# Performance work log

Hardware: AMD Instinct MI355X
Metric: run time of the kernel (lower is better)

The kernel has to match this reference:

```python
import jax, jax.numpy as jnp
import numpy as np

N = 100000; E = 1600000; G = 256
DIMS = [16, 64, 128, 128, 64]
HEADS = 4


def _self_loops(edge_index, n):
    loop = jnp.arange(n, dtype=edge_index.dtype)
    row = jnp.concatenate([edge_index[0], loop])  # source nodes j
    col = jnp.concatenate([edge_index[1], loop])  # target nodes i (aggregation index)
    return row, col


def _gcn(x, row, col, W, b, n):
    deg = jax.ops.segment_sum(jnp.ones_like(col, jnp.float32), col, num_segments=n)
    dis = jax.lax.rsqrt(deg)  # self-loops guarantee deg >= 1
    norm = dis[row] * dis[col]  # [E+N]
    h = x @ W  # [N, dout]
    return jax.ops.segment_sum(h[row] * norm[:, None], col, num_segments=n) + b


def _gat(x, row, col, W, a_src, a_dst, b, n):
    # PyG GATConv with self-loops; per-edge softmax over incoming neighborhoods.
    H, C = a_src.shape
    h = (x @ W).reshape(n, H, C)
    asrc = jnp.einsum('nhc,hc->nh', h, a_src)
    adst = jnp.einsum('nhc,hc->nh', h, a_dst)
    e = jax.nn.leaky_relu(asrc[row] + adst[col], 0.2)  # [E+N, H]
    m = jax.ops.segment_max(e, col, num_segments=n)
    ex = jnp.exp(e - m[col])
    s = jax.ops.segment_sum(ex, col, num_segments=n)
    alpha = ex / s[col]  # segment softmax over edges sharing a target
    out = jax.ops.segment_sum(h[row] * alpha[..., None], col, num_segments=n)
    return out.reshape(n, H * C) + b  # heads concatenated so residual add is valid


def _bn(x, g, b):
    # BatchNorm1d training-mode normalization (biased variance), eps=1e-5
    mu = jnp.mean(x, 0)
    var = jnp.var(x, 0)
    return (x - mu) * jax.lax.rsqrt(var + 1e-5) * g + b


def _forward(x, edge_index, batch, p):
    row, col = _self_loops(edge_index, N)
    gat_at = {0: 0, 2: 1}  # layers 0 and 2 have attention (i % 2 == 0 and i < n-1)
    n_layers = len(DIMS) - 1
    for i in range(n_layers):
        x = _gcn(x, row, col, p['gcn_w'][i], p['gcn_b'][i], N)
        x = _bn(x, p['bn_g'][i], p['bn_b'][i])
        if i in gat_at:
            j = gat_at[i]
            x = _gat(x, row, col, p['gat_w'][j], p['gat_asrc'][j], p['gat_adst'][j], p['gat_b'][j], N) + x
        if i < n_layers - 1:
            x = jax.nn.leaky_relu(x, 0.2)
            # dropout: identity in eval mode
    sums = jax.ops.segment_sum(x, batch, num_segments=G)
    cnt = jax.ops.segment_sum(jnp.ones((N,), jnp.float32), batch, num_segments=G)
    return sums / jnp.maximum(cnt, 1.0)[:, None]  # global_mean_pool -> [G, latent]


def setup_inputs() -> dict:
    key = jax.random.key(0)
    ks = jax.random.split(key, 16)
    inp = {}
    inp['x'] = jax.random.normal(ks[0], (N, DIMS[0]), jnp.float32)
    inp['edge_index'] = jax.random.randint(ks[1], (2, E), 0, N, dtype=jnp.int32)
    inp['batch'] = jnp.sort(jax.random.randint(ks[2], (N,), 0, G, dtype=jnp.int32))
    k = 3
    for i in range(4):
        din, dout = DIMS[i], DIMS[i + 1]
        inp[f'gcn_w{i}'] = jax.random.normal(ks[k], (din, dout), jnp.float32) / np.sqrt(din).astype(np.float32); k += 1
        inp[f'gcn_b{i}'] = jnp.zeros((dout,), jnp.float32)
        inp[f'bn_g{i}'] = jnp.ones((dout,), jnp.float32)
        inp[f'bn_b{i}'] = jnp.zeros((dout,), jnp.float32)
    for i in (0, 2):
        d = DIMS[i + 1]; C = d // HEADS
        inp[f'gat_w{i}'] = jax.random.normal(ks[k], (d, d), jnp.float32) / np.sqrt(d).astype(np.float32); k += 1
        inp[f'gat_asrc{i}'] = jax.random.normal(ks[k], (HEADS, C), jnp.float32) * 0.1; k += 1
        inp[f'gat_adst{i}'] = jax.random.normal(ks[k], (HEADS, C), jnp.float32) * 0.1; k += 1
        inp[f'gat_b{i}'] = jnp.zeros((d,), jnp.float32)
    return inp


def reference(x, edge_index, batch,
              gcn_w0, gcn_b0, bn_g0, bn_b0,
              gcn_w1, gcn_b1, bn_g1, bn_b1,
              gcn_w2, gcn_b2, bn_g2, bn_b2,
              gcn_w3, gcn_b3, bn_g3, bn_b3,
              gat_w0, gat_asrc0, gat_adst0, gat_b0,
              gat_w2, gat_asrc2, gat_adst2, gat_b2):
    p = {
        'gcn_w': [gcn_w0, gcn_w1, gcn_w2, gcn_w3],
        'gcn_b': [gcn_b0, gcn_b1, gcn_b2, gcn_b3],
        'bn_g': [bn_g0, bn_g1, bn_g2, bn_g3],
        'bn_b': [bn_b0, bn_b1, bn_b2, bn_b3],
        'gat_w': [gat_w0, gat_w2],
        'gat_asrc': [gat_asrc0, gat_asrc2],
        'gat_adst': [gat_adst0, gat_adst2],
        'gat_b': [gat_b0, gat_b2],
    }
    return _forward(x, edge_index, batch, p)
```

## Files before the change

kernel.cpp:

```cpp
#include <hip/hip_runtime.h>

static constexpr int GRAPHS = 256;
static constexpr int SCAN_CHUNK = 1024;
static constexpr int XCDS = 8;
static constexpr int SREP = 8;

typedef _Float16 h16;
typedef _Float16 h16x2 __attribute__((ext_vector_type(2)));
typedef _Float16 h16x4 __attribute__((ext_vector_type(4)));
typedef _Float16 v8h __attribute__((ext_vector_type(8)));
typedef float v4f __attribute__((ext_vector_type(4)));

__device__ __forceinline__ float lrelu(float v) { return fmaxf(v, 0.2f * v); }
__device__ __forceinline__ int rfl(int v) { return __builtin_amdgcn_readfirstlane(v); }

__global__ void zero_f32_kernel(float* __restrict__ p, int n) {
  int i = blockIdx.x * blockDim.x + threadIdx.x;
  if (i < n) p[i] = 0.0f;
}

__global__ void init_counts_kernel(int* __restrict__ cnt, int n) {
  int i = blockIdx.x * blockDim.x + threadIdx.x;
  if (i < n) cnt[i] = 1;
}

__global__ void count_edges_kernel(const int* __restrict__ ei, int* __restrict__ cnt, int E) {
  int e = blockIdx.x * blockDim.x + threadIdx.x;
  if (e < E) atomicAdd(&cnt[ei[E + e]], 1);
}

__global__ void block_sum_kernel(const int* __restrict__ counts, int* __restrict__ partial,
                                 int n) {
  __shared__ int sh[256];
  int base = blockIdx.x * SCAN_CHUNK;
  int t = threadIdx.x;
  int lim = min(base + SCAN_CHUNK, n);
  int s = 0;
  for (int i = base + t; i < lim; i += 256) s += counts[i];
  sh[t] = s;
  __syncthreads();
  for (int off = 128; off > 0; off >>= 1) {
    if (t < off) sh[t] += sh[t + off];
    __syncthreads();
  }
  if (t == 0) partial[blockIdx.x] = sh[0];
}

__global__ void partial_scan_kernel(int* __restrict__ partial, int* __restrict__ rowptr,
                                    int nblocks, int n) {
  __shared__ int sh[256];
  int t = threadIdx.x;
  int v = (t < nblocks) ? partial[t] : 0;
  sh[t] = v;
  __syncthreads();
  for (int off = 1; off < 256; off <<= 1) {
    int u = (t >= off) ? sh[t - off] : 0;
    __syncthreads();
    sh[t] += u;
    __syncthreads();
  }
  if (t < nblocks) partial[t] = sh[t] - v;
  if (t == 255) rowptr[n] = sh[255];
}

__global__ void chunk_scan_kernel(const int* __restrict__ counts, const int* __restrict__ partial,
                                  int* __restrict__ rowptr, int n) {
  __shared__ int sh[256];
  int base = blockIdx.x * SCAN_CHUNK;
  int t = threadIdx.x;
  int i0 = base + t * 4;
  int c0 = 0, c1 = 0, c2 = 0, c3 = 0;
  if (i0 + 3 < n) {
    int4 c = *(const int4*)(counts + i0);
    c0 = c.x;
    c1 = c.y;
    c2 = c.z;
    c3 = c.w;
  } else {
    if (i0 < n) c0 = counts[i0];
    if (i0 + 1 < n) c1 = counts[i0 + 1];
    if (i0 + 2 < n) c2 = counts[i0 + 2];
  }
  int tot = c0 + c1 + c2 + c3;
  sh[t] = tot;
  __syncthreads();
  for (int off = 1; off < 256; off <<= 1) {
    int u = (t >= off) ? sh[t - off] : 0;
    __syncthreads();
    sh[t] += u;
    __syncthreads();
  }
  int run = partial[blockIdx.x] + sh[t] - tot;
  if (i0 < n) { rowptr[i0] = run; run += c0; }
  if (i0 + 1 < n) { rowptr[i0 + 1] = run; run += c1; }
  if (i0 + 2 < n) { rowptr[i0 + 2] = run; run += c2; }
  if (i0 + 3 < n) { rowptr[i0 + 3] = run; }
}

__global__ void finalize_csr_kernel(const int* __restrict__ rowptr, float* __restrict__ dis,
                                    int* __restrict__ cursor, int* __restrict__ csr, int n) {
  int i = blockIdx.x * blockDim.x + threadIdx.x;
  if (i >= n) return;
  int s = rowptr[i], e = rowptr[i + 1];
  dis[i] = rsqrtf((float)(e - s));
  csr[s] = i;
  cursor[i] = s + 1;
}

__global__ void fill_edges_kernel(const int* __restrict__ ei, int* __restrict__ cursor,
                                  int* __restrict__ csr, int E, int nb) {
  int p = blockIdx.x & (XCDS - 1);
  int lo = p * nb, hi = lo + nb;
  int nchunks = gridDim.x >> 3;
  int chunk = blockIdx.x >> 3;
  int stride = nchunks * blockDim.x;
  for (int e = chunk * blockDim.x + threadIdx.x; e < E; e += stride) {
    int c = ei[E + e];
    if (c >= lo && c < hi) {
      int pos = atomicAdd(&cursor[c], 1);
      csr[pos] = ei[e];
    }
  }
}

template <int K, int N>
__global__ void wt_kernel(const float* __restrict__ W, h16* __restrict__ WT) {
  int gid = blockIdx.x * blockDim.x + threadIdx.x;
  if (gid >= K * N) return;
  int k = gid / N, n = gid % N;
  WT[n * K + k] = (h16)W[gid];
}

template <int K, int N, bool STATS>
__global__ void gemm_mfma_kernel(const h16* __restrict__ x, const h16* __restrict__ WT,
                                 const float* __restrict__ bias, const float* __restrict__ coefIn,
                                 h16* __restrict__ out, double* __restrict__ stats, int n_nodes) {
  constexpr int KP = K + 8;
  constexpr int NT = N / 16;
  __shared__ h16 Ah[128 * KP];
  __shared__ h16 Bs[N * KP];
  __shared__ float sh1[N], sh2[N];
  int tid = threadIdx.x;
  int node0 = blockIdx.x * 128;
  int limit = min(128, n_nodes - node0);
  if (STATS && tid < N) {
    sh1[tid] = 0.f;
    sh2[tid] = 0.f;
  }
  for (int i = tid; i < 128 * (K / 8); i += 256) {
    int row = i / (K / 8), kb = i % (K / 8);
    v8h v = {};
    if (row < limit) {
      v = *(const v8h*)(x + (size_t)(node0 + row) * K + kb * 8);
      if (coefIn) {
#pragma unroll
        for (int j = 0; j < 8; ++j)
          v[j] = (h16)fmaf((float)v[j], coefIn[kb * 8 + j], coefIn[K + kb * 8 + j]);
      }
    }
    *(v8h*)(Ah + row * KP + kb * 8) = v;
  }
  for (int i = tid; i < N * (K / 8); i += 256) {
    int nrow = i / (K / 8), kb = i % (K / 8);
    *(v8h*)(Bs + nrow * KP + kb * 8) = *(const v8h*)(WT + (size_t)nrow * K + kb * 8);
  }
  __syncthreads();

  int w = tid >> 6, lane = tid & 63, quad = lane >> 4, l16 = lane & 15;
  v4f acc[2][NT];
#pragma unroll
  for (int rt = 0; rt < 2; ++rt)
#pragma unroll
    for (int nt = 0; nt < NT; ++nt) acc[rt][nt] = (v4f){0.f, 0.f, 0.f, 0.f};

  int rowb = w * 32;
#pragma unroll
  for (int ks = 0; ks < K / 32; ++ks) {
    v8h a0 = *(const v8h*)(Ah + (rowb + l16) * KP + ks * 32 + quad * 8);
    v8h a1 = *(const v8h*)(Ah + (rowb + 16 + l16) * KP + ks * 32 + quad * 8);
#pragma unroll
    for (int nt = 0; nt < NT; ++nt) {
      v8h b = *(const v8h*)(Bs + (nt * 16 + l16) * KP + ks * 32 + quad * 8);
      acc[0][nt] = __builtin_amdgcn_mfma_f32_16x16x32_f16(a0, b, acc[0][nt], 0, 0, 0);
      acc[1][nt] = __builtin_amdgcn_mfma_f32_16x16x32_f16(a1, b, acc[1][nt], 0, 0, 0);
    }
  }

#pragma unroll
  for (int nt = 0; nt < NT; ++nt) {
    int col = nt * 16 + l16;
    float bv = bias ? bias[col] : 0.f;
    float p1 = 0.f, p2 = 0.f;
#pragma unroll
    for (int rt = 0; rt < 2; ++rt) {
#pragma unroll
      for (int reg = 0; reg < 4; ++reg) {
        int row = rowb + rt * 16 + quad * 4 + reg;
        if (row < limit) {
          float v = acc[rt][nt][reg] + bv;
          out[(size_t)(node0 + row) * N + col] = (h16)v;
          if (STATS) {
            p1 += v;
            p2 = fmaf(v, v, p2);
          }
        }
      }
    }
    if (STATS) {
      atomicAdd(&sh1[col], p1);
      atomicAdd(&sh2[col], p2);
    }
  }
  if (STATS) {
    __syncthreads();
    double* st = stats + (blockIdx.x & (SREP - 1)) * 256;
    if (tid < N) {
      atomicAdd(&st[tid], (double)sh1[tid]);
      atomicAdd(&st[N + tid], (double)sh2[tid]);
    }
  }
}

template <int K, int DOUT, int MT, bool STATS>
__global__ void gemm_tile_kernel(const h16* __restrict__ x, const float* __restrict__ W,
                                 const float* __restrict__ bias, h16* __restrict__ out,
                                 double* __restrict__ stats, int n_nodes) {
  constexpr int COLG = DOUT / 4;
  constexpr int ROWG = 256 / COLG;
  constexpr int NODES = ROWG * MT;
  constexpr int KP = K + 4;
  __shared__ float xs[NODES * KP];
  __shared__ float sh1[DOUT], sh2[DOUT];
  int tid = threadIdx.x;
  if (STATS && tid < DOUT) {
    sh1[tid] = 0.f;
    sh2[tid] = 0.f;
  }
  int node0 = blockIdx.x * NODES;
  int limit = min(NODES, n_nodes - node0);
  const h16x4* src = (const h16x4*)(x + (size_t)node0 * K);
  int tile_q = (limit * K) >> 2;
  for (int i = tid; i < tile_q; i += 256) {
    h16x4 v = src[i];
    int row = i / (K / 4), cq = i % (K / 4);
    float4 f;
    f.x = (float)v[0];
    f.y = (float)v[1];
    f.z = (float)v[2];
    f.w = (float)v[3];
    *(float4*)(xs + row * KP + cq * 4) = f;
  }
  __syncthreads();
  int cg = tid % COLG, rg = tid / COLG;
  int c0 = cg * 4;
  float acc[MT][4];
#pragma unroll
  for (int m = 0; m < MT; ++m)
#pragma unroll
    for (int i = 0; i < 4; ++i) acc[m][i] = 0.f;

  for (int k4 = 0; k4 < K / 4; ++k4) {
    int k = k4 * 4;
    float4 w0 = *(const float4*)(W + (size_t)(k + 0) * DOUT + c0);
    float4 w1 = *(const float4*)(W + (size_t)(k + 1) * DOUT + c0);
    float4 w2 = *(const float4*)(W + (size_t)(k + 2) * DOUT + c0);
    float4 w3 = *(const float4*)(W + (size_t)(k + 3) * DOUT + c0);
#pragma unroll
    for (int m = 0; m < MT; ++m) {
      float4 xv = *(const float4*)(xs + (rg * MT + m) * KP + k);
      acc[m][0] = fmaf(xv.x, w0.x, acc[m][0]);
      acc[m][1] = fmaf(xv.x, w0.y, acc[m][1]);
      acc[m][2] = fmaf(xv.x, w0.z, acc[m][2]);
      acc[m][3] = fmaf(xv.x, w0.w, acc[m][3]);
      acc[m][0] = fmaf(xv.y, w1.x, acc[m][0]);
      acc[m][1] = fmaf(xv.y, w1.y, acc[m][1]);
      acc[m][2] = fmaf(xv.y, w1.z, acc[m][2]);
      acc[m][3] = fmaf(xv.y, w1.w, acc[m][3]);
      acc[m][0] = fmaf(xv.z, w2.x, acc[m][0]);
      acc[m][1] = fmaf(xv.z, w2.y, acc[m][1]);
      acc[m][2] = fmaf(xv.z, w2.z, acc[m][2]);
      acc[m][3] = fmaf(xv.z, w2.w, acc[m][3]);
      acc[m][0] = fmaf(xv.w, w3.x, acc[m][0]);
      acc[m][1] = fmaf(xv.w, w3.y, acc[m][1]);
      acc[m][2] = fmaf(xv.w, w3.z, acc[m][2]);
      acc[m][3] = fmaf(xv.w, w3.w, acc[m][3]);
    }
  }
  float4 bv = make_float4(0.f, 0.f, 0.f, 0.f);
  if (bias) bv = *(const float4*)(bias + c0);
  float p1[4] = {0.f, 0.f, 0.f, 0.f}, p2[4] = {0.f, 0.f, 0.f, 0.f};
#pragma unroll
  for (int m = 0; m < MT; ++m) {
    int node = node0 + rg * MT + m;
    if (node < n_nodes) {
      float v0 = acc[m][0] + bv.x, v1 = acc[m][1] + bv.y;
      float v2 = acc[m][2] + bv.z, v3 = acc[m][3] + bv.w;
      h16x4 r;
      r[0] = (h16)v0;
      r[1] = (h16)v1;
      r[2] = (h16)v2;
      r[3] = (h16)v3;
      *(h16x4*)(out + (size_t)node * DOUT + c0) = r;
      if (STATS) {
        p1[0] += v0;
        p1[1] += v1;
        p1[2] += v2;
        p1[3] += v3;
        p2[0] = fmaf(v0, v0, p2[0]);
        p2[1] = fmaf(v1, v1, p2[1]);
        p2[2] = fmaf(v2, v2, p2[2]);
        p2[3] = fmaf(v3, v3, p2[3]);
      }
    }
  }
  if (STATS) {
#pragma unroll
    for (int i = 0; i < 4; ++i) {
      atomicAdd(&sh1[c0 + i], p1[i]);
      atomicAdd(&sh2[c0 + i], p2[i]);
    }
    __syncthreads();
    double* st = stats + (blockIdx.x & (SREP - 1)) * 256;
    if (tid < DOUT) {
      atomicAdd(&st[tid], (double)sh1[tid]);
      atomicAdd(&st[DOUT + tid], (double)sh2[tid]);
    }
  }
}

template <int D>
__global__ void bn_stats_kernel(const h16* __restrict__ x, double* __restrict__ stats, int n) {
  int tid = threadIdx.x;
  int c = tid & (D - 1);
  const int rpb = 256 / D;
  float s1 = 0.f, s2 = 0.f;
  for (int r = blockIdx.x * rpb + tid / D; r < n; r += gridDim.x * rpb) {
    float v = (float)x[(size_t)r * D + c];
    s1 += v;
    s2 = fmaf(v, v, s2);
  }
  double* st = stats + (blockIdx.x & (SREP - 1)) * 256;
  atomicAdd(&st[c], (double)s1);
  atomicAdd(&st[D + c], (double)s2);
}

template <int D>
__global__ void bn_coef_kernel(const double* __restrict__ stats, const float* __restrict__ g,
                               const float* __restrict__ b, float* __restrict__ coef, int n) {
  int c = threadIdx.x;
  if (c >= D) return;
  double s1 = 0.0, s2 = 0.0;
#pragma unroll
  for (int r = 0; r < SREP; ++r) {
    s1 += stats[r * 256 + c];
    s2 += stats[r * 256 + D + c];
  }
  double inv_n = 1.0 / (double)n;
  double mu = s1 * inv_n;
  double var = s2 * inv_n - mu * mu;
  float A = (float)(1.0 / sqrt(var + 1e-5)) * g[c];
  coef[c] = A;
  coef[D + c] = b[c] - (float)mu * A;
}

__global__ void gcn_agg16_kernel(const float* __restrict__ h, const int* __restrict__ rowptr,
                                 const int* __restrict__ csr, const float* __restrict__ dis,
                                 h16* __restrict__ out, int n) {
  int wave = (blockIdx.x * blockDim.x + threadIdx.x) >> 6;
  int lane = threadIdx.x & 63;
  if (wave >= n) return;
  int s = rowptr[wave], e = rowptr[wave + 1];
  int q = lane >> 4, c = lane & 15;
  float acc = 0.f;
  for (int k = s + q; k < e; k += 4) {
    int j = csr[k];
    acc = fmaf(dis[j], h[(size_t)j * 16 + c], acc);
  }
  acc += __shfl_xor(acc, 16, 64);
  acc += __shfl_xor(acc, 32, 64);
  if (lane < 16) out[(size_t)wave * 16 + lane] = (h16)(dis[wave] * acc);
}

__global__ void gcn_agg64_kernel(const h16* __restrict__ h, const int* __restrict__ rowptr,
                                 const int* __restrict__ csr, const float* __restrict__ dis,
                                 const float* __restrict__ bias, h16* __restrict__ out, int n) {
  int wave = (blockIdx.x * blockDim.x + threadIdx.x) >> 6;
  int lane = threadIdx.x & 63;
  if (wave >= n) return;
  int s = rfl(rowptr[wave]);
  int e = rfl(rowptr[wave + 1]);
  float a[4] = {0.f, 0.f, 0.f, 0.f};
  int k = s;
  for (; k + 8 <= e; k += 8) {
    int j[8];
    float d[8];
#pragma unroll
    for (int u = 0; u < 8; ++u) j[u] = rfl(csr[k + u]);
#pragma unroll
    for (int u = 0; u < 8; ++u) d[u] = dis[j[u]];
#pragma unroll
    for (int u = 0; u < 8; ++u) {
      const h16* rp = h + (size_t)j[u] * 64;
      a[u & 3] = fmaf(d[u], (float)rp[lane], a[u & 3]);
    }
  }
  for (; k + 4 <= e; k += 4) {
    int j[4];
#pragma unroll
    for (int u = 0; u < 4; ++u) j[u] = rfl(csr[k + u]);
#pragma unroll
    for (int u = 0; u < 4; ++u) {
      const h16* rp = h + (size_t)j[u] * 64;
      a[u] = fmaf(dis[j[u]], (float)rp[lane], a[u]);
    }
  }
  for (; k < e; ++k) {
    int j0 = rfl(csr[k]);
    const h16* rp = h + (size_t)j0 * 64;
    a[0] = fmaf(dis[j0], (float)rp[lane], a[0]);
  }
  float b0 = bias ? bias[lane] : 0.f;
  out[(size_t)wave * 64 + lane] = (h16)fmaf(dis[wave], (a[0] + a[1]) + (a[2] + a[3]), b0);
}

template <bool COEF>
__global__ void gcn_agg128_kernel(const h16* __restrict__ h, const int* __restrict__ rowptr,
                                  const int* __restrict__ csr, const float* __restrict__ dis,
                                  const float* __restrict__ coef, h16* __restrict__ out, int n) {
  int wave = (blockIdx.x * blockDim.x + threadIdx.x) >> 6;
  int lane = threadIdx.x & 63;
  if (wave >= n) return;
  int s = rfl(rowptr[wave]);
  int e = rfl(rowptr[wave + 1]);
  int c2 = lane * 2;
  float2 A2 = make_float2(0.f, 0.f), B2 = make_float2(0.f, 0.f);
  if (COEF) {
    A2 = *(const float2*)(coef + c2);
    B2 = *(const float2*)(coef + 128 + c2);
  }
  float a0[4] = {0.f, 0.f, 0.f, 0.f};
  float a1[4] = {0.f, 0.f, 0.f, 0.f};
  int k = s;
  for (; k + 8 <= e; k += 8) {
    int j[8];
    float d[8];
#pragma unroll
    for (int u = 0; u < 8; ++u) j[u] = rfl(csr[k + u]);
#pragma unroll
    for (int u = 0; u < 8; ++u) d[u] = dis[j[u]];
#pragma unroll
    for (int u = 0; u < 8; ++u) {
      const h16* rp = h + (size_t)j[u] * 128;
      h16x2 v = *(const h16x2*)(rp + c2);
      float f0 = (float)v[0], f1 = (float)v[1];
      if (COEF) {
        f0 = lrelu(fmaf(f0, A2.x, B2.x));
        f1 = lrelu(fmaf(f1, A2.y, B2.y));
      }
      a0[u & 3] = fmaf(d[u], f0, a0[u & 3]);
      a1[u & 3] = fmaf(d[u], f1, a1[u & 3]);
    }
  }
  for (; k < e; ++k) {
    int j0 = rfl(csr[k]);
    float d0 = dis[j0];
    const h16* rp = h + (size_t)j0 * 128;
    h16x2 v = *(const h16x2*)(rp + c2);
    float f0 = (float)v[0], f1 = (float)v[1];
    if (COEF) {
      f0 = lrelu(fmaf(f0, A2.x, B2.x));
      f1 = lrelu(fmaf(f1, A2.y, B2.y));
    }
    a0[0] = fmaf(d0, f0, a0[0]);
    a1[0] = fmaf(d0, f1, a1[0]);
  }
  float di = dis[wave];
  h16x2 r;
  r[0] = (h16)(di * ((a0[0] + a0[1]) + (a0[2] + a0[3])));
  r[1] = (h16)(di * ((a1[0] + a1[1]) + (a1[2] + a1[3])));
  *(h16x2*)(out + (size_t)wave * 128 + c2) = r;
}

template <int C>
__global__ void att_coef_kernel(const h16* __restrict__ h2, const float* __restrict__ a_src,
                                const float* __restrict__ a_dst, float* __restrict__ asrc,
                                float* __restrict__ adst, int n) {
  int gid = blockIdx.x * blockDim.x + threadIdx.x;
  if (gid >= n * 4) return;
  int nd = gid >> 2, h = gid & 3;
  const h16* hr = h2 + (size_t)nd * 4 * C + h * C;
  float s1 = 0.f, s2 = 0.f;
#pragma unroll
  for (int c = 0; c < C; ++c) {
    float v = (float)hr[c];
    s1 = fmaf(v, a_src[h * C + c], s1);
    s2 = fmaf(v, a_dst[h * C + c], s2);
  }
  asrc[gid] = s1;
  adst[gid] = s2;
}

__global__ void edge_coef_kernel(const int* __restrict__ rowptr, const int* __restrict__ csr,
                                 const float* __restrict__ asrc, const float* __restrict__ adst,
                                 float* __restrict__ exbuf, float* __restrict__ dinv, int n) {
  int wave = (blockIdx.x * blockDim.x + threadIdx.x) >> 6;
  int lane = threadIdx.x & 63;
  if (wave >= n) return;
  int h = lane & 3, es = lane >> 2;
  float ad = adst[wave * 4 + h];
  int s = rowptr[wave], e = rowptr[wave + 1];
  float den = 0.f;
  for (int k = s + es; k < e; k += 16) {
    int j = csr[k];
    float v = __expf(lrelu(asrc[j * 4 + h] + ad));
    exbuf[(size_t)k * 4 + h] = v;
    den += v;
  }
  den += __shfl_xor(den, 4, 64);
  den += __shfl_xor(den, 8, 64);
  den += __shfl_xor(den, 16, 64);
  den += __shfl_xor(den, 32, 64);
  if (lane < 4) dinv[wave * 4 + h] = 1.0f / den;
}

__global__ void gat_agg64_kernel(const h16* __restrict__ h2, const int* __restrict__ rowptr,
                                 const int* __restrict__ csr, const float* __restrict__ exbuf,
                                 const float* __restrict__ dinv, const float* __restrict__ bias,
                                 const h16* __restrict__ xres, const float* __restrict__ rescoef,
                                 h16* __restrict__ out, int n) {
  int wave = (blockIdx.x * blockDim.x + threadIdx.x) >> 6;
  int lane = threadIdx.x & 63;
  if (wave >= n) return;
  int head = lane >> 4;
  int s = rfl(rowptr[wave]);
  int e = rfl(rowptr[wave + 1]);
  float a[4] = {0.f, 0.f, 0.f, 0.f};
  int k = s;
  for (; k + 8 <= e; k += 8) {
    int j[8];
    float ex[8];
#pragma unroll
    for (int u = 0; u < 8; ++u) {
      j[u] = rfl(csr[k + u]);
      ex[u] = exbuf[(size_t)(k + u) * 4 + head];
    }
#pragma unroll
    for (int u = 0; u < 8; ++u) {
      const h16* rp = h2 + (size_t)j[u] * 64;
      a[u & 3] = fmaf(ex[u], (float)rp[lane], a[u & 3]);
    }
  }
  for (; k + 4 <= e; k += 4) {
    int j[4];
    float ex[4];
#pragma unroll
    for (int u = 0; u < 4; ++u) {
      j[u] = rfl(csr[k + u]);
      ex[u] = exbuf[(size_t)(k + u) * 4 + head];
    }
#pragma unroll
    for (int u = 0; u < 4; ++u) {
      const h16* rp = h2 + (size_t)j[u] * 64;
      a[u] = fmaf(ex[u], (float)rp[lane], a[u]);
    }
  }
  for (; k < e; ++k) {
    int j0 = rfl(csr[k]);
    const h16* rp = h2 + (size_t)j0 * 64;
    a[0] = fmaf(exbuf[(size_t)k * 4 + head], (float)rp[lane], a[0]);
  }
  float dv = dinv[wave * 4 + head];
  size_t base = (size_t)wave * 64;
  float xv = fmaf((float)xres[base + lane], rescoef[lane], rescoef[64 + lane]);
  float v0 = ((a[0] + a[1]) + (a[2] + a[3])) * dv + bias[lane] + xv;
  out[base + lane] = (h16)lrelu(v0);
}

__global__ void gat_agg128_kernel(const h16* __restrict__ h2, const int* __restrict__ rowptr,
                                  const int* __restrict__ csr, const float* __restrict__ exbuf,
                                  const float* __restrict__ dinv, const float* __restrict__ bias,
                                  const h16* __restrict__ xres, const float* __restrict__ rescoef,
                                  h16* __restrict__ out, int n) {
  int wave = (blockIdx.x * blockDim.x + threadIdx.x) >> 6;
  int lane = threadIdx.x & 63;
  if (wave >= n) return;
  int head = lane >> 4;
  int c2 = lane * 2;
  int s = rfl(rowptr[wave]);
  int e = rfl(rowptr[wave + 1]);
  float a0[4] = {0.f, 0.f, 0.f, 0.f};
  float a1[4] = {0.f, 0.f, 0.f, 0.f};
  int k = s;
  for (; k + 8 <= e; k += 8) {
    int j[8];
    float ex[8];
#pragma unroll
    for (int u = 0; u < 8; ++u) {
      j[u] = rfl(csr[k + u]);
      ex[u] = exbuf[(size_t)(k + u) * 4 + head];
    }
#pragma unroll
    for (int u = 0; u < 8; ++u) {
      const h16* rp = h2 + (size_t)j[u] * 128;
      h16x2 v = *(const h16x2*)(rp + c2);
      a0[u & 3] = fmaf(ex[u], (float)v[0], a0[u & 3]);
      a1[u & 3] = fmaf(ex[u], (float)v[1], a1[u & 3]);
    }
  }
  for (; k + 4 <= e; k += 4) {
    int j[4];
    float ex[4];
#pragma unroll
    for (int u = 0; u < 4; ++u) {
      j[u] = rfl(csr[k + u]);
      ex[u] = exbuf[(size_t)(k + u) * 4 + head];
    }
#pragma unroll
    for (int u = 0; u < 4; ++u) {
      const h16* rp = h2 + (size_t)j[u] * 128;
      h16x2 v = *(const h16x2*)(rp + c2);
      a0[u] = fmaf(ex[u], (float)v[0], a0[u]);
      a1[u] = fmaf(ex[u], (float)v[1], a1[u]);
    }
  }
  for (; k < e; ++k) {
    int j0 = rfl(csr[k]);
    float e0 = exbuf[(size_t)k * 4 + head];
    const h16* rp = h2 + (size_t)j0 * 128;
    h16x2 v = *(const h16x2*)(rp + c2);
    a0[0] = fmaf(e0, (float)v[0], a0[0]);
    a1[0] = fmaf(e0, (float)v[1], a1[0]);
  }
  float dv = dinv[wave * 4 + head];
  float2 b2 = *(const float2*)(bias + c2);
  float2 A2 = *(const float2*)(rescoef + c2);
  float2 B2 = *(const float2*)(rescoef + 128 + c2);
  size_t base = (size_t)wave * 128;
  h16x2 xr = *(const h16x2*)(xres + base + c2);
  float xr0 = fmaf((float)xr[0], A2.x, B2.x);
  float xr1 = fmaf((float)xr[1], A2.y, B2.y);
  float v0 = ((a0[0] + a0[1]) + (a0[2] + a0[3])) * dv + b2.x + xr0;
  float v1 = ((a1[0] + a1[1]) + (a1[2] + a1[3])) * dv + b2.y + xr1;
  h16x2 r;
  r[0] = (h16)lrelu(v0);
  r[1] = (h16)lrelu(v1);
  *(h16x2*)(out + base + c2) = r;
}

__global__ void graph_bounds_kernel(const int* __restrict__ batch, int* __restrict__ bounds,
                                    int n) {
  int g = threadIdx.x;
  if (g >= GRAPHS) return;
  int lo = 0, hi = n;
  while (lo < hi) {
    int mid = (lo + hi) >> 1;
    if (batch[mid] < g)
      lo = mid + 1;
    else
      hi = mid;
  }
  bounds[g] = lo;
  if (g == 0) bounds[GRAPHS] = n;
}

__global__ void pool_kernel(const h16* __restrict__ x, const int* __restrict__ bounds,
                            const float* __restrict__ coef, float* __restrict__ out) {
  __shared__ float sh[4][64];
  int g = blockIdx.x;
  int lane = threadIdx.x & 63, w = threadIdx.x >> 6;
  int s = bounds[g], e = bounds[g + 1];
  float acc = 0.f;
  for (int r = s + w; r < e; r += 4) acc += (float)x[(size_t)r * 64 + lane];
  sh[w][lane] = acc;
  __syncthreads();
  if (w == 0) {
    float t = sh[0][lane] + sh[1][lane] + sh[2][lane] + sh[3][lane];
    float cntf = (float)(e - s);
    out[(g << 6) + lane] = fmaf(coef[lane], t, coef[64 + lane] * cntf) / fmaxf(cntf, 1.0f);
  }
}

extern "C" void kernel_launch(void* const* d_in, const int* in_sizes, int n_in, void* d_out,
                              int out_size, void* d_ws, size_t ws_size, hipStream_t stream) {
  const float* x_in = (const float*)d_in[0];
  const int* ei = (const int*)d_in[1];
  const int* batch = (const int*)d_in[2];
  const float* gcn_w[4] = {(const float*)d_in[3], (const float*)d_in[7], (const float*)d_in[11],
                           (const float*)d_in[15]};
  const float* gcn_b[4] = {(const float*)d_in[4], (const float*)d_in[8], (const float*)d_in[12],
                           (const float*)d_in[16]};
  const float* bn_g[4] = {(const float*)d_in[5], (const float*)d_in[9], (const float*)d_in[13],
                          (const float*)d_in[17]};
  const float* bn_b[4] = {(const float*)d_in[6], (const float*)d_in[10], (const float*)d_in[14],
                          (const float*)d_in[18]};
  const float* gat_w0 = (const float*)d_in[19];
  const float* gat_as0 = (const float*)d_in[20];
  const float* gat_ad0 = (const float*)d_in[21];
  const float* gat_b0 = (const float*)d_in[22];
  const float* gat_w2 = (const float*)d_in[23];
  const float* gat_as2 = (const float*)d_in[24];
  const float* gat_ad2 = (const float*)d_in[25];
  const float* gat_b2 = (const float*)d_in[26];

  const int N = in_sizes[2];
  const int E = in_sizes[1] / 2;

  char* wp = (char*)d_ws;
  auto alloc = [&](size_t bytes) -> void* {
    void* p = (void*)wp;
    wp += (bytes + 255) & ~(size_t)255;
    return p;
  };
  double* statsAll = (double*)alloc(4 * SREP * 256 * sizeof(double));
  float* coefAll = (float*)alloc(4 * 256 * sizeof(float));
  int* rowptr = (int*)alloc((size_t)(N + 1) * 4);
  int* cursor = (int*)alloc((size_t)N * 4);
  int* partial = (int*)alloc(256 * sizeof(int));
  int* csr = (int*)alloc((size_t)(N + E) * 4);
  float* dis = (float*)alloc((size_t)N * 4);
  h16* bufA = (h16*)alloc((size_t)N * 128 * 2);
  h16* bufB = (h16*)alloc((size_t)N * 128 * 2);
  h16* bufC = (h16*)alloc((size_t)N * 128 * 2);
  float* attS = (float*)alloc((size_t)N * 4 * 4);
  float* attD = (float*)alloc((size_t)N * 4 * 4);
  float* exbuf = (float*)alloc((size_t)(N + E) * 4 * 4);
  float* dinv = (float*)alloc((size_t)N * 4 * 4);
  int* bounds = (int*)alloc((size_t)(GRAPHS + 1) * 4);
  h16* wt0 = (h16*)alloc(64 * 64 * 2);
  h16* wt1 = (h16*)alloc(64 * 128 * 2);
  h16* wt2 = (h16*)alloc(128 * 128 * 2);
  h16* wt3 = (h16*)alloc(128 * 128 * 2);
  h16* wt4 = (h16*)alloc(128 * 64 * 2);
  if ((size_t)(wp - (char*)d_ws) > ws_size) return;

  double* stats0 = statsAll;
  double* stats1 = statsAll + SREP * 256;
  double* stats2 = statsAll + 2 * SREP * 256;
  double* stats3 = statsAll + 3 * SREP * 256;
  float* coef0 = coefAll;
  float* coef1 = coefAll + 256;
  float* coef2 = coefAll + 512;
  float* coef3 = coefAll + 768;

  const int B = 256;
  auto cd = [](int a, int b) { return (a + b - 1) / b; };
  const int scan_blocks = cd(N, SCAN_CHUNK);

  zero_f32_kernel<<<cd(4 * SREP * 512, B), B, 0, stream>>>((float*)statsAll, 4 * SREP * 512);
  wt_kernel<64, 64><<<cd(64 * 64, B), B, 0, stream>>>(gat_w0, wt0);
  wt_kernel<64, 128><<<cd(64 * 128, B), B, 0, stream>>>(gcn_w[1], wt1);
  wt_kernel<128, 128><<<cd(128 * 128, B), B, 0, stream>>>(gcn_w[2], wt2);
  wt_kernel<128, 128><<<cd(128 * 128, B), B, 0, stream>>>(gat_w2, wt3);
  wt_kernel<128, 64><<<cd(128 * 64, B), B, 0, stream>>>(gcn_w[3], wt4);
  init_counts_kernel<<<cd(N, B), B, 0, stream>>>(cursor, N);
  count_edges_kernel<<<cd(E, B), B, 0, stream>>>(ei, cursor, E);
  block_sum_kernel<<<scan_blocks, B, 0, stream>>>(cursor, partial, N);
  partial_scan_kernel<<<1, B, 0, stream>>>(partial, rowptr, scan_blocks, N);
  chunk_scan_kernel<<<scan_blocks, B, 0, stream>>>(cursor, partial, rowptr, N);
  finalize_csr_kernel<<<cd(N, B), B, 0, stream>>>(rowptr, dis, cursor, csr, N);
  {
    int nb = cd(N, XCDS);
    fill_edges_kernel<<<XCDS * 512, B, 0, stream>>>(ei, cursor, csr, E, nb);
  }
  graph_bounds_kernel<<<1, 256, 0, stream>>>(batch, bounds, N);

  gcn_agg16_kernel<<<cd(N * 64, B), B, 0, stream>>>(x_in, rowptr, csr, dis, bufB, N);
  gemm_tile_kernel<16, 64, 8, true>
      <<<cd(N, 128), B, 0, stream>>>(bufB, gcn_w[0], gcn_b[0], bufC, stats0, N);
  bn_coef_kernel<64><<<1, 64, 0, stream>>>(stats0, bn_g[0], bn_b[0], coef0, N);
  gemm_mfma_kernel<64, 64, false>
      <<<cd(N, 128), B, 0, stream>>>(bufC, wt0, nullptr, coef0, bufB, nullptr, N);
  att_coef_kernel<16><<<cd(N * 4, B), B, 0, stream>>>(bufB, gat_as0, gat_ad0, attS, attD, N);
  edge_coef_kernel<<<cd(N * 64, B), B, 0, stream>>>(rowptr, csr, attS, attD, exbuf, dinv, N);
  gat_agg64_kernel<<<cd(N * 64, B), B, 0, stream>>>(bufB, rowptr, csr, exbuf, dinv, gat_b0, bufC,
                                                    coef0, bufA, N);

  gcn_agg64_kernel<<<cd(N * 64, B), B, 0, stream>>>(bufA, rowptr, csr, dis, nullptr, bufB, N);
  gemm_mfma_kernel<64, 128, true>
      <<<cd(N, 128), B, 0, stream>>>(bufB, wt1, gcn_b[1], nullptr, bufC, stats1, N);
  bn_coef_kernel<128><<<1, 128, 0, stream>>>(stats1, bn_g[1], bn_b[1], coef1, N);

  gcn_agg128_kernel<true><<<cd(N * 64, B), B, 0, stream>>>(bufC, rowptr, csr, dis, coef1, bufB, N);
  gemm_mfma_kernel<128, 128, true>
      <<<cd(N, 128), B, 0, stream>>>(bufB, wt2, gcn_b[2], nullptr, bufA, stats2, N);
  bn_coef_kernel<128><<<1, 128, 0, stream>>>(stats2, bn_g[2], bn_b[2], coef2, N);
  gemm_mfma_kernel<128, 128, false>
      <<<cd(N, 128), B, 0, stream>>>(bufA, wt3, nullptr, coef2, bufB, nullptr, N);
  att_coef_kernel<32><<<cd(N * 4, B), B, 0, stream>>>(bufB, gat_as2, gat_ad2, attS, attD, N);
  edge_coef_kernel<<<cd(N * 64, B), B, 0, stream>>>(rowptr, csr, attS, attD, exbuf, dinv, N);
  gat_agg128_kernel<<<cd(N * 64, B), B, 0, stream>>>(bufB, rowptr, csr, exbuf, dinv, gat_b2, bufA,
                                                     coef2, bufC, N);

  gemm_mfma_kernel<128, 64, false>
      <<<cd(N, 128), B, 0, stream>>>(bufC, wt4, nullptr, nullptr, bufB, nullptr, N);
  gcn_agg64_kernel<<<cd(N * 64, B), B, 0, stream>>>(bufB, rowptr, csr, dis, gcn_b[3], bufA, N);
  bn_stats_kernel<64><<<256, 256, 0, stream>>>(bufA, stats3, N);
  bn_coef_kernel<64><<<1, 64, 0, stream>>>(stats3, bn_g[3], bn_b[3], coef3, N);

  pool_kernel<<<GRAPHS, 256, 0, stream>>>(bufA, bounds, coef3, (float*)d_out);
}
```

Measured before the change: 915.8 us.

## Fuse GAT edge softmax into aggregation and bucket edges by target partition

Removes the separate edge_coef kernel and its exbuf/dinv buffers. Each GAT aggregation wave now computes the exp-scores for 8 edges at once across 32 lanes, broadcasts them with shuffles, and accumulates the softmax denominator inline. CSR construction now first partitions edges into 8 target-range buckets through a histogram, prefix and scatter, so the count and fill atomics touch only a contiguous slice per XCD instead of each partition rescanning all edges. This avoids writing and rereading the per-edge coefficient buffer and the 8x redundant edge-list scans, at the cost of an extra scatter pass through an 8-byte-per-edge staging buffer.

```diff
diff --git a/kernel.cpp b/kernel.cpp
--- a/kernel.cpp
+++ b/kernel.cpp
@@ -24,9 +24,64 @@
   if (i < n) cnt[i] = 1;
 }
 
-__global__ void count_edges_kernel(const int* __restrict__ ei, int* __restrict__ cnt, int E) {
-  int e = blockIdx.x * blockDim.x + threadIdx.x;
-  if (e < E) atomicAdd(&cnt[ei[E + e]], 1);
+__global__ void bucket_hist_kernel(const int* __restrict__ ei, int* __restrict__ bcnt, int E,
+                                   int nbkt) {
+  __shared__ int h[8];
+  if (threadIdx.x < 8) h[threadIdx.x] = 0;
+  __syncthreads();
+  int stride = gridDim.x * blockDim.x;
+  for (int e = blockIdx.x * blockDim.x + threadIdx.x; e < E; e += stride)
+    atomicAdd(&h[ei[E + e] / nbkt], 1);
+  __syncthreads();
+  if (threadIdx.x < 8) atomicAdd(&bcnt[threadIdx.x], h[threadIdx.x]);
+}
+
+__global__ void bucket_prefix_kernel(const int* __restrict__ bcnt, int* __restrict__ bstart,
+                                     int* __restrict__ bcursor) {
+  int run = 0;
+  for (int i = 0; i < 8; ++i) {
+    bstart[i] = run;
+    bcursor[i] = run;
+    run += bcnt[i];
+  }
+  bstart[8] = run;
+}
+
+__global__ void bucket_scatter_kernel(const int* __restrict__ ei, int* __restrict__ bcursor,
+                                      int2* __restrict__ ebuf, int E, int nbkt) {
+  constexpr int EPT = 8;
+  __shared__ int h[8], base[8];
+  int tid = threadIdx.x;
+  if (tid < 8) h[tid] = 0;
+  __syncthreads();
+  int base_e = blockIdx.x * (256 * EPT);
+  int src[EPT], tgt[EPT], bk[EPT], rnk[EPT];
+#pragma unroll
+  for (int i = 0; i < EPT; ++i) {
+    int e = base_e + i * 256 + tid;
+    bk[i] = -1;
+    if (e < E) {
+      tgt[i] = ei[E + e];
+      src[i] = ei[e];
+      bk[i] = tgt[i] / nbkt;
+      rnk[i] = atomicAdd(&h[bk[i]], 1);
+    }
+  }
+  __syncthreads();
+  if (tid < 8) base[tid] = atomicAdd(&bcursor[tid], h[tid]);
+  __syncthreads();
+#pragma unroll
+  for (int i = 0; i < EPT; ++i)
+    if (bk[i] >= 0) ebuf[base[bk[i]] + rnk[i]] = make_int2(src[i], tgt[i]);
+}
+
+__global__ void count_bucket_kernel(const int2* __restrict__ ebuf, const int* __restrict__ bstart,
+                                    int* __restrict__ cnt) {
+  int p = blockIdx.x & (XCDS - 1);
+  int s = bstart[p], e = bstart[p + 1];
+  int ch = blockIdx.x >> 3, nch = gridDim.x >> 3;
+  int stride = nch * 256;
+  for (int i = s + ch * 256 + threadIdx.x; i < e; i += stride) atomicAdd(&cnt[ebuf[i].y], 1);
 }
 
 __global__ void block_sum_kernel(const int* __restrict__ counts, int* __restrict__ partial,
@@ -107,19 +162,16 @@
   cursor[i] = s + 1;
 }
 
-__global__ void fill_edges_kernel(const int* __restrict__ ei, int* __restrict__ cursor,
-                                  int* __restrict__ csr, int E, int nb) {
+__global__ void fill_bucket_kernel(const int2* __restrict__ ebuf, const int* __restrict__ bstart,
+                                   int* __restrict__ cursor, int* __restrict__ csr) {
   int p = blockIdx.x & (XCDS - 1);
-  int lo = p * nb, hi = lo + nb;
-  int nchunks = gridDim.x >> 3;
-  int chunk = blockIdx.x >> 3;
-  int stride = nchunks * blockDim.x;
-  for (int e = chunk * blockDim.x + threadIdx.x; e < E; e += stride) {
-    int c = ei[E + e];
-    if (c >= lo && c < hi) {
-      int pos = atomicAdd(&cursor[c], 1);
-      csr[pos] = ei[e];
-    }
+  int s = bstart[p], e = bstart[p + 1];
+  int ch = blockIdx.x >> 3, nch = gridDim.x >> 3;
+  int stride = nch * 256;
+  for (int i = s + ch * 256 + threadIdx.x; i < e; i += stride) {
+    int2 st = ebuf[i];
+    int pos = atomicAdd(&cursor[st.y], 1);
+    csr[pos] = st.x;
   }
 }
 
@@ -500,85 +552,54 @@
   adst[gid] = s2;
 }
 
-__global__ void edge_coef_kernel(const int* __restrict__ rowptr, const int* __restrict__ csr,
-                                 const float* __restrict__ asrc, const float* __restrict__ adst,
-                                 float* __restrict__ exbuf, float* __restrict__ dinv, int n) {
-  int wave = (blockIdx.x * blockDim.x + threadIdx.x) >> 6;
-  int lane = threadIdx.x & 63;
-  if (wave >= n) return;
-  int h = lane & 3, es = lane >> 2;
-  float ad = adst[wave * 4 + h];
-  int s = rowptr[wave], e = rowptr[wave + 1];
-  float den = 0.f;
-  for (int k = s + es; k < e; k += 16) {
-    int j = csr[k];
-    float v = __expf(lrelu(asrc[j * 4 + h] + ad));
-    exbuf[(size_t)k * 4 + h] = v;
-    den += v;
-  }
-  den += __shfl_xor(den, 4, 64);
-  den += __shfl_xor(den, 8, 64);
-  den += __shfl_xor(den, 16, 64);
-  den += __shfl_xor(den, 32, 64);
-  if (lane < 4) dinv[wave * 4 + h] = 1.0f / den;
-}
-
 __global__ void gat_agg64_kernel(const h16* __restrict__ h2, const int* __restrict__ rowptr,
-                                 const int* __restrict__ csr, const float* __restrict__ exbuf,
-                                 const float* __restrict__ dinv, const float* __restrict__ bias,
+                                 const int* __restrict__ csr, const float* __restrict__ asrc,
+                                 const float* __restrict__ adst, const float* __restrict__ bias,
                                  const h16* __restrict__ xres, const float* __restrict__ rescoef,
                                  h16* __restrict__ out, int n) {
   int wave = (blockIdx.x * blockDim.x + threadIdx.x) >> 6;
   int lane = threadIdx.x & 63;
   if (wave >= n) return;
   int head = lane >> 4;
+  float ad_sub = adst[wave * 4 + (lane & 3)];
+  float ad_head = adst[wave * 4 + head];
   int s = rfl(rowptr[wave]);
   int e = rfl(rowptr[wave + 1]);
   float a[4] = {0.f, 0.f, 0.f, 0.f};
+  float ss = 0.f;
   int k = s;
   for (; k + 8 <= e; k += 8) {
+    float exv = 0.f;
+    if (lane < 32) {
+      int jj = csr[k + (lane >> 2)];
+      exv = __expf(lrelu(asrc[jj * 4 + (lane & 3)] + ad_sub));
+    }
     int j[8];
-    float ex[8];
+#pragma unroll
+    for (int u = 0; u < 8; ++u) j[u] = rfl(csr[k + u]);
 #pragma unroll
     for (int u = 0; u < 8; ++u) {
-      j[u] = rfl(csr[k + u]);
-      ex[u] = exbuf[(size_t)(k + u) * 4 + head];
-    }
-#pragma unroll
-    for (int u = 0; u < 8; ++u) {
+      float exu = __shfl(exv, u * 4 + head, 64);
+      ss += exu;
       const h16* rp = h2 + (size_t)j[u] * 64;
-      a[u & 3] = fmaf(ex[u], (float)rp[lane], a[u & 3]);
-    }
-  }
-  for (; k + 4 <= e; k += 4) {
-    int j[4];
-    float ex[4];
-#pragma unroll
-    for (int u = 0; u < 4; ++u) {
-      j[u] = rfl(csr[k + u]);
-      ex[u] = exbuf[(size_t)(k + u) * 4 + head];
-    }
-#pragma unroll
-    for (int u = 0; u < 4; ++u) {
-      const h16* rp = h2 + (size_t)j[u] * 64;
-      a[u] = fmaf(ex[u], (float)rp[lane], a[u]);
+      a[u & 3] = fmaf(exu, (float)rp[lane], a[u & 3]);
     }
   }
   for (; k < e; ++k) {
     int j0 = rfl(csr[k]);
-    const h16* rp = h2 + (size_t)j0 * 64;
-    a[0] = fmaf(exbuf[(size_t)k * 4 + head], (float)rp[lane], a[0]);
-  }
-  float dv = dinv[wave * 4 + head];
+    float ex0 = __expf(lrelu(asrc[j0 * 4 + head] + ad_head));
+    ss += ex0;
+    a[0] = fmaf(ex0, (float)h2[(size_t)j0 * 64 + lane], a[0]);
+  }
   size_t base = (size_t)wave * 64;
   float xv = fmaf((float)xres[base + lane], rescoef[lane], rescoef[64 + lane]);
-  float v0 = ((a[0] + a[1]) + (a[2] + a[3])) * dv + bias[lane] + xv;
+  float v0 = ((a[0] + a[1]) + (a[2] + a[3])) / ss + bias[lane] + xv;
   out[base + lane] = (h16)lrelu(v0);
 }
 
 __global__ void gat_agg128_kernel(const h16* __restrict__ h2, const int* __restrict__ rowptr,
-                                  const int* __restrict__ csr, const float* __restrict__ exbuf,
-                                  const float* __restrict__ dinv, const float* __restrict__ bias,
+                                  const int* __restrict__ csr, const float* __restrict__ asrc,
+                                  const float* __restrict__ adst, const float* __restrict__ bias,
                                   const h16* __restrict__ xres, const float* __restrict__ rescoef,
                                   h16* __restrict__ out, int n) {
   int wave = (blockIdx.x * blockDim.x + threadIdx.x) >> 6;
@@ -586,52 +607,43 @@
   if (wave >= n) return;
   int head = lane >> 4;
   int c2 = lane * 2;
+  float ad_sub = adst[wave * 4 + (lane & 3)];
+  float ad_head = adst[wave * 4 + head];
   int s = rfl(rowptr[wave]);
   int e = rfl(rowptr[wave + 1]);
   float a0[4] = {0.f, 0.f, 0.f, 0.f};
   float a1[4] = {0.f, 0.f, 0.f, 0.f};
+  float ss = 0.f;
   int k = s;
   for (; k + 8 <= e; k += 8) {
+    float exv = 0.f;
+    if (lane < 32) {
+      int jj = csr[k + (lane >> 2)];
+      exv = __expf(lrelu(asrc[jj * 4 + (lane & 3)] + ad_sub));
+    }
     int j[8];
-    float ex[8];
+#pragma unroll
+    for (int u = 0; u < 8; ++u) j[u] = rfl(csr[k + u]);
 #pragma unroll
     for (int u = 0; u < 8; ++u) {
-      j[u] = rfl(csr[k + u]);
-      ex[u] = exbuf[(size_t)(k + u) * 4 + head];
-    }
-#pragma unroll
-    for (int u = 0; u < 8; ++u) {
+      float exu = __shfl(exv, u * 4 + head, 64);
+      ss += exu;
       const h16* rp = h2 + (size_t)j[u] * 128;
       h16x2 v = *(const h16x2*)(rp + c2);
-      a0[u & 3] = fmaf(ex[u], (float)v[0], a0[u & 3]);
-      a1[u & 3] = fmaf(ex[u], (float)v[1], a1[u & 3]);
-    }
-  }
-  for (; k + 4 <= e; k += 4) {
-    int j[4];
-    float ex[4];
-#pragma unroll
-    for (int u = 0; u < 4; ++u) {
-      j[u] = rfl(csr[k + u]);
-      ex[u] = exbuf[(size_t)(k + u) * 4 + head];
-    }
-#pragma unroll
-    for (int u = 0; u < 4; ++u) {
-      const h16* rp = h2 + (size_t)j[u] * 128;
-      h16x2 v = *(const h16x2*)(rp + c2);
-      a0[u] = fmaf(ex[u], (float)v[0], a0[u]);
-      a1[u] = fmaf(ex[u], (float)v[1], a1[u]);
+      a0[u & 3] = fmaf(exu, (float)v[0], a0[u & 3]);
+      a1[u & 3] = fmaf(exu, (float)v[1], a1[u & 3]);
     }
   }
   for (; k < e; ++k) {
     int j0 = rfl(csr[k]);
-    float e0 = exbuf[(size_t)k * 4 + head];
+    float ex0 = __expf(lrelu(asrc[j0 * 4 + head] + ad_head));
+    ss += ex0;
     const h16* rp = h2 + (size_t)j0 * 128;
     h16x2 v = *(const h16x2*)(rp + c2);
-    a0[0] = fmaf(e0, (float)v[0], a0[0]);
-    a1[0] = fmaf(e0, (float)v[1], a1[0]);
-  }
-  float dv = dinv[wave * 4 + head];
+    a0[0] = fmaf(ex0, (float)v[0], a0[0]);
+    a1[0] = fmaf(ex0, (float)v[1], a1[0]);
+  }
+  float dv = 1.0f / ss;
   float2 b2 = *(const float2*)(bias + c2);
   float2 A2 = *(const float2*)(rescoef + c2);
   float2 B2 = *(const float2*)(rescoef + 128 + c2);
@@ -716,15 +728,15 @@
   int* rowptr = (int*)alloc((size_t)(N + 1) * 4);
   int* cursor = (int*)alloc((size_t)N * 4);
   int* partial = (int*)alloc(256 * sizeof(int));
+  int* bmeta = (int*)alloc(32 * sizeof(int));
   int* csr = (int*)alloc((size_t)(N + E) * 4);
+  int2* ebuf = (int2*)alloc((size_t)E * 8);
   float* dis = (float*)alloc((size_t)N * 4);
   h16* bufA = (h16*)alloc((size_t)N * 128 * 2);
   h16* bufB = (h16*)alloc((size_t)N * 128 * 2);
   h16* bufC = (h16*)alloc((size_t)N * 128 * 2);
   float* attS = (float*)alloc((size_t)N * 4 * 4);
   float* attD = (float*)alloc((size_t)N * 4 * 4);
-  float* exbuf = (float*)alloc((size_t)(N + E) * 4 * 4);
-  float* dinv = (float*)alloc((size_t)N * 4 * 4);
   int* bounds = (int*)alloc((size_t)(GRAPHS + 1) * 4);
   h16* wt0 = (h16*)alloc(64 * 64 * 2);
   h16* wt1 = (h16*)alloc(64 * 128 * 2);
@@ -732,6 +744,10 @@
   h16* wt3 = (h16*)alloc(128 * 128 * 2);
   h16* wt4 = (h16*)alloc(128 * 64 * 2);
   if ((size_t)(wp - (char*)d_ws) > ws_size) return;
+
+  int* bcnt = bmeta;
+  int* bstart = bmeta + 8;
+  int* bcursor = bmeta + 17;
 
   double* stats0 = statsAll;
   double* stats1 = statsAll + SREP * 256;
@@ -745,23 +761,25 @@
   const int B = 256;
   auto cd = [](int a, int b) { return (a + b - 1) / b; };
   const int scan_blocks = cd(N, SCAN_CHUNK);
+  const int nbkt = cd(N, XCDS);
 
   zero_f32_kernel<<<cd(4 * SREP * 512, B), B, 0, stream>>>((float*)statsAll, 4 * SREP * 512);
+  zero_f32_kernel<<<1, 32, 0, stream>>>((float*)bmeta, 32);
   wt_kernel<64, 64><<<cd(64 * 64, B), B, 0, stream>>>(gat_w0, wt0);
   wt_kernel<64, 128><<<cd(64 * 128, B), B, 0, stream>>>(gcn_w[1], wt1);
   wt_kernel<128, 128><<<cd(128 * 128, B), B, 0, stream>>>(gcn_w[2], wt2);
   wt_kernel<128, 128><<<cd(128 * 128, B), B, 0, stream>>>(gat_w2, wt3);
   wt_kernel<128, 64><<<cd(128 * 64, B), B, 0, stream>>>(gcn_w[3], wt4);
   init_counts_kernel<<<cd(N, B), B, 0, stream>>>(cursor, N);
-  count_edges_kernel<<<cd(E, B), B, 0, stream>>>(ei, cursor, E);
+  bucket_hist_kernel<<<1024, B, 0, stream>>>(ei, bcnt, E, nbkt);
+  bucket_prefix_kernel<<<1, 1, 0, stream>>>(bcnt, bstart, bcursor);
+  bucket_scatter_kernel<<<cd(E, 2048), B, 0, stream>>>(ei, bcursor, ebuf, E, nbkt);
+  count_bucket_kernel<<<XCDS * 256, B, 0, stream>>>(ebuf, bstart, cursor);
   block_sum_kernel<<<scan_blocks, B, 0, stream>>>(cursor, partial, N);
   partial_scan_kernel<<<1, B, 0, stream>>>(partial, rowptr, scan_blocks, N);
   chunk_scan_kernel<<<scan_blocks, B, 0, stream>>>(cursor, partial, rowptr, N);
   finalize_csr_kernel<<<cd(N, B), B, 0, stream>>>(rowptr, dis, cursor, csr, N);
-  {
-    int nb = cd(N, XCDS);
-    fill_edges_kernel<<<XCDS * 512, B, 0, stream>>>(ei, cursor, csr, E, nb);
-  }
+  fill_bucket_kernel<<<XCDS * 256, B, 0, stream>>>(ebuf, bstart, cursor, csr);
   graph_bounds_kernel<<<1, 256, 0, stream>>>(batch, bounds, N);
 
   gcn_agg16_kernel<<<cd(N * 64, B), B, 0, stream>>>(x_in, rowptr, csr, dis, bufB, N);
@@ -771,8 +789,7 @@
   gemm_mfma_kernel<64, 64, false>
       <<<cd(N, 128), B, 0, stream>>>(bufC, wt0, nullptr, coef0, bufB, nullptr, N);
   att_coef_kernel<16><<<cd(N * 4, B), B, 0, stream>>>(bufB, gat_as0, gat_ad0, attS, attD, N);
-  edge_coef_kernel<<<cd(N * 64, B), B, 0, stream>>>(rowptr, csr, attS, attD, exbuf, dinv, N);
-  gat_agg64_kernel<<<cd(N * 64, B), B, 0, stream>>>(bufB, rowptr, csr, exbuf, dinv, gat_b0, bufC,
+  gat_agg64_kernel<<<cd(N * 64, B), B, 0, stream>>>(bufB, rowptr, csr, attS, attD, gat_b0, bufC,
                                                     coef0, bufA, N);
 
   gcn_agg64_kernel<<<cd(N * 64, B), B, 0, stream>>>(bufA, rowptr, csr, dis, nullptr, bufB, N);
@@ -787,8 +804,7 @@
   gemm_mfma_kernel<128, 128, false>
       <<<cd(N, 128), B, 0, stream>>>(bufA, wt3, nullptr, coef2, bufB, nullptr, N);
   att_coef_kernel<32><<<cd(N * 4, B), B, 0, stream>>>(bufB, gat_as2, gat_ad2, attS, attD, N);
-  edge_coef_kernel<<<cd(N * 64, B), B, 0, stream>>>(rowptr, csr, attS, attD, exbuf, dinv, N);
-  gat_agg128_kernel<<<cd(N * 64, B), B, 0, stream>>>(bufB, rowptr, csr, exbuf, dinv, gat_b2, bufA,
+  gat_agg128_kernel<<<cd(N * 64, B), B, 0, stream>>>(bufB, rowptr, csr, attS, attD, gat_b2, bufA,
                                                      coef2, bufC, N);
 
   gemm_mfma_kernel<128, 64, false>
```

Measured after the change: 924.6 us. About the same (+1.0%).

## Pre-bucket edges by target partition before CSR count and fill

Applied to the files above, without the earlier changes.

Replaces the direct count and XCD-partitioned fill passes with a bucket pipeline. A histogram, a prefix step and a scatter place the (src,tgt) pairs into 8 contiguous target-range buckets. The count and fill kernels then each read only their own bucket, so atomics stay local to an XCD and each fill pass no longer rescans the whole edge list. It also merges the five weight-transpose launches into one. The cost is an extra edge-buffer write and read plus three more small kernels.

```diff
diff --git a/kernel.cpp b/kernel.cpp
--- a/kernel.cpp
+++ b/kernel.cpp
@@ -19,14 +19,70 @@
   if (i < n) p[i] = 0.0f;
 }
 
-__global__ void init_counts_kernel(int* __restrict__ cnt, int n) {
+__global__ void init_counts_kernel(int* __restrict__ cnt, int* __restrict__ bmeta, int n) {
   int i = blockIdx.x * blockDim.x + threadIdx.x;
   if (i < n) cnt[i] = 1;
-}
-
-__global__ void count_edges_kernel(const int* __restrict__ ei, int* __restrict__ cnt, int E) {
-  int e = blockIdx.x * blockDim.x + threadIdx.x;
-  if (e < E) atomicAdd(&cnt[ei[E + e]], 1);
+  if (i < 32) bmeta[i] = 0;
+}
+
+__global__ void bucket_hist_kernel(const int* __restrict__ ei, int* __restrict__ bcnt, int E,
+                                   int nbkt) {
+  __shared__ int h[8];
+  if (threadIdx.x < 8) h[threadIdx.x] = 0;
+  __syncthreads();
+  int stride = gridDim.x * blockDim.x;
+  for (int e = blockIdx.x * blockDim.x + threadIdx.x; e < E; e += stride)
+    atomicAdd(&h[ei[E + e] / nbkt], 1);
+  __syncthreads();
+  if (threadIdx.x < 8) atomicAdd(&bcnt[threadIdx.x], h[threadIdx.x]);
+}
+
+__global__ void bucket_prefix_kernel(const int* __restrict__ bcnt, int* __restrict__ bstart,
+                                     int* __restrict__ bcursor) {
+  int run = 0;
+  for (int i = 0; i < 8; ++i) {
+    bstart[i] = run;
+    bcursor[i] = run;
+    run += bcnt[i];
+  }
+  bstart[8] = run;
+}
+
+__global__ void bucket_scatter_kernel(const int* __restrict__ ei, int* __restrict__ bcursor,
+                                      int2* __restrict__ ebuf, int E, int nbkt) {
+  constexpr int EPT = 8;
+  __shared__ int h[8], base[8];
+  int tid = threadIdx.x;
+  if (tid < 8) h[tid] = 0;
+  __syncthreads();
+  int base_e = blockIdx.x * (256 * EPT);
+  int src[EPT], tgt[EPT], bk[EPT], rnk[EPT];
+#pragma unroll
+  for (int i = 0; i < EPT; ++i) {
+    int e = base_e + i * 256 + tid;
+    bk[i] = -1;
+    if (e < E) {
+      tgt[i] = ei[E + e];
+      src[i] = ei[e];
+      bk[i] = tgt[i] / nbkt;
+      rnk[i] = atomicAdd(&h[bk[i]], 1);
+    }
+  }
+  __syncthreads();
+  if (tid < 8) base[tid] = atomicAdd(&bcursor[tid], h[tid]);
+  __syncthreads();
+#pragma unroll
+  for (int i = 0; i < EPT; ++i)
+    if (bk[i] >= 0) ebuf[base[bk[i]] + rnk[i]] = make_int2(src[i], tgt[i]);
+}
+
+__global__ void count_bucket_kernel(const int2* __restrict__ ebuf, const int* __restrict__ bstart,
+                                    int* __restrict__ cnt) {
+  int p = blockIdx.x & (XCDS - 1);
+  int s = bstart[p], e = bstart[p + 1];
+  int ch = blockIdx.x >> 3, nch = gridDim.x >> 3;
+  int stride = nch * 256;
+  for (int i = s + ch * 256 + threadIdx.x; i < e; i += stride) atomicAdd(&cnt[ebuf[i].y], 1);
 }
 
 __global__ void block_sum_kernel(const int* __restrict__ counts, int* __restrict__ partial,
@@ -107,28 +163,45 @@
   cursor[i] = s + 1;
 }
 
-__global__ void fill_edges_kernel(const int* __restrict__ ei, int* __restrict__ cursor,
-                                  int* __restrict__ csr, int E, int nb) {
+__global__ void fill_bucket_kernel(const int2* __restrict__ ebuf, const int* __restrict__ bstart,
+                                   int* __restrict__ cursor, int* __restrict__ csr) {
   int p = blockIdx.x & (XCDS - 1);
-  int lo = p * nb, hi = lo + nb;
-  int nchunks = gridDim.x >> 3;
-  int chunk = blockIdx.x >> 3;
-  int stride = nchunks * blockDim.x;
-  for (int e = chunk * blockDim.x + threadIdx.x; e < E; e += stride) {
-    int c = ei[E + e];
-    if (c >= lo && c < hi) {
-      int pos = atomicAdd(&cursor[c], 1);
-      csr[pos] = ei[e];
-    }
-  }
-}
-
-template <int K, int N>
-__global__ void wt_kernel(const float* __restrict__ W, h16* __restrict__ WT) {
+  int s = bstart[p], e = bstart[p + 1];
+  int ch = blockIdx.x >> 3, nch = gridDim.x >> 3;
+  int stride = nch * 256;
+  for (int i = s + ch * 256 + threadIdx.x; i < e; i += stride) {
+    int2 st = ebuf[i];
+    int pos = atomicAdd(&cursor[st.y], 1);
+    csr[pos] = st.x;
+  }
+}
+
+__global__ void wt_all_kernel(const float* __restrict__ w0, const float* __restrict__ w1,
+                              const float* __restrict__ w2, const float* __restrict__ w3,
+                              const float* __restrict__ w4, h16* __restrict__ t0,
+                              h16* __restrict__ t1, h16* __restrict__ t2, h16* __restrict__ t3,
+                              h16* __restrict__ t4) {
   int gid = blockIdx.x * blockDim.x + threadIdx.x;
-  if (gid >= K * N) return;
-  int k = gid / N, n = gid % N;
-  WT[n * K + k] = (h16)W[gid];
+  if (gid < 4096) {
+    int k = gid / 64, n = gid % 64;
+    t0[n * 64 + k] = (h16)w0[gid];
+  } else if (gid < 12288) {
+    int i = gid - 4096;
+    int k = i / 128, n = i % 128;
+    t1[n * 64 + k] = (h16)w1[i];
+  } else if (gid < 28672) {
+    int i = gid - 12288;
+    int k = i / 128, n = i % 128;
+    t2[n * 128 + k] = (h16)w2[i];
+  } else if (gid < 45056) {
+    int i = gid - 28672;
+    int k = i / 128, n = i % 128;
+    t3[n * 128 + k] = (h16)w3[i];
+  } else if (gid < 53248) {
+    int i = gid - 45056;
+    int k = i / 64, n = i % 64;
+    t4[n * 128 + k] = (h16)w4[i];
+  }
 }
 
 template <int K, int N, bool STATS>
@@ -716,7 +789,9 @@
   int* rowptr = (int*)alloc((size_t)(N + 1) * 4);
   int* cursor = (int*)alloc((size_t)N * 4);
   int* partial = (int*)alloc(256 * sizeof(int));
+  int* bmeta = (int*)alloc(32 * sizeof(int));
   int* csr = (int*)alloc((size_t)(N + E) * 4);
+  int2* ebuf = (int2*)alloc((size_t)E * 8);
   float* dis = (float*)alloc((size_t)N * 4);
   h16* bufA = (h16*)alloc((size_t)N * 128 * 2);
   h16* bufB = (h16*)alloc((size_t)N * 128 * 2);
@@ -733,6 +808,10 @@
   h16* wt4 = (h16*)alloc(128 * 64 * 2);
   if ((size_t)(wp - (char*)d_ws) > ws_size) return;
 
+  int* bcnt = bmeta;
+  int* bstart = bmeta + 8;
+  int* bcursor = bmeta + 17;
+
   double* stats0 = statsAll;
   double* stats1 = statsAll + SREP * 256;
   double* stats2 = statsAll + 2 * SREP * 256;
@@ -745,23 +824,21 @@
   const int B = 256;
   auto cd = [](int a, int b) { return (a + b - 1) / b; };
   const int scan_blocks = cd(N, SCAN_CHUNK);
+  const int nbkt = cd(N, XCDS);
 
   zero_f32_kernel<<<cd(4 * SREP * 512, B), B, 0, stream>>>((float*)statsAll, 4 * SREP * 512);
-  wt_kernel<64, 64><<<cd(64 * 64, B), B, 0, stream>>>(gat_w0, wt0);
-  wt_kernel<64, 128><<<cd(64 * 128, B), B, 0, stream>>>(gcn_w[1], wt1);
-  wt_kernel<128, 128><<<cd(128 * 128, B), B, 0, stream>>>(gcn_w[2], wt2);
-  wt_kernel<128, 128><<<cd(128 * 128, B), B, 0, stream>>>(gat_w2, wt3);
-  wt_kernel<128, 64><<<cd(128 * 64, B), B, 0, stream>>>(gcn_w[3], wt4);
-  init_counts_kernel<<<cd(N, B), B, 0, stream>>>(cursor, N);
-  count_edges_kernel<<<cd(E, B), B, 0, stream>>>(ei, cursor, E);
+  wt_all_kernel<<<cd(53248, B), B, 0, stream>>>(gat_w0, gcn_w[1], gcn_w[2], gat_w2, gcn_w[3], wt0,
+                                                wt1, wt2, wt3, wt4);
+  init_counts_kernel<<<cd(N, B), B, 0, stream>>>(cursor, bmeta, N);
+  bucket_hist_kernel<<<1024, B, 0, stream>>>(ei, bcnt, E, nbkt);
+  bucket_prefix_kernel<<<1, 1, 0, stream>>>(bcnt, bstart, bcursor);
+  bucket_scatter_kernel<<<cd(E, 2048), B, 0, stream>>>(ei, bcursor, ebuf, E, nbkt);
+  count_bucket_kernel<<<XCDS * 256, B, 0, stream>>>(ebuf, bstart, cursor);
   block_sum_kernel<<<scan_blocks, B, 0, stream>>>(cursor, partial, N);
   partial_scan_kernel<<<1, B, 0, stream>>>(partial, rowptr, scan_blocks, N);
   chunk_scan_kernel<<<scan_blocks, B, 0, stream>>>(cursor, partial, rowptr, N);
   finalize_csr_kernel<<<cd(N, B), B, 0, stream>>>(rowptr, dis, cursor, csr, N);
-  {
-    int nb = cd(N, XCDS);
-    fill_edges_kernel<<<XCDS * 512, B, 0, stream>>>(ei, cursor, csr, E, nb);
-  }
+  fill_bucket_kernel<<<XCDS * 256, B, 0, stream>>>(ebuf, bstart, cursor, csr);
   graph_bounds_kernel<<<1, 256, 0, stream>>>(batch, bounds, N);
 
   gcn_agg16_kernel<<<cd(N * 64, B), B, 0, stream>>>(x_in, rowptr, csr, dis, bufB, N);
```

New measurement: 941.3 us. 2.8% more time.
